# Kernel tuning notes

Measured on AMD Instinct MI355X. Metric: run time of the kernel, lower is better.

## Reference

```python
import jax, jax.numpy as jnp
import numpy as np

N = 30000      # nodes
E = 480000     # edges
H = 128        # hidden_nf
NQ = 7         # qubits
D = 2 ** NQ    # 128, quantum state dim == embedding_size
NL = 2         # block n_layers (QGCL layers)
QL = 2         # quantum circuit layers inside each QGCL
NORM = 100.0   # normalization_factor ('sum' aggregation)
NORM_CONST = 1.0


def _cnot_perm_indices(n):
    # Composed permutation for CNOT(0,1)...CNOT(n-2,n-1), CNOT(n-1,0).
    # PennyLane convention: wire 0 is the most significant bit.
    idx = np.arange(2 ** n)
    pairs = [(i, i + 1) for i in range(n - 1)] + [(n - 1, 0)]
    g = None
    for c, t in pairs:
        cb = (idx >> (n - 1 - c)) & 1
        f = idx ^ (cb << (n - 1 - t))  # flip target bit if control set (involution)
        g = f if g is None else g[f]
    return g

_CNOT_G = jnp.asarray(_cnot_perm_indices(NQ))


def _quantum_states(q_in, coeffs, A_re, A_im):
    """Vectorized VQC over all nodes. q_in [N,D] real -> [N,D] complex state."""
    norm = jnp.sqrt(jnp.sum(q_in ** 2, axis=1, keepdims=True) + 1e-12)
    s = (q_in / norm).astype(jnp.complex64)  # normalized initial state per node
    I = jnp.eye(D, dtype=jnp.complex64)
    for j in range(QL):
        # Cayley transform -> unitary
        A = (A_re[j] + 1j * A_im[j]).astype(jnp.complex64)
        A = A + A.conj().T
        q = (A - 1j * I) @ jnp.linalg.inv(A + 1j * I)
        # single-qubit layer: RY(b) @ RX(a) on every qubit -> kron power
        a, b = coeffs[j, 0].astype(jnp.complex64), coeffs[j, 1].astype(jnp.complex64)
        ca, sa = jnp.cos(a / 2), jnp.sin(a / 2)
        cb, sb = jnp.cos(b / 2), jnp.sin(b / 2)
        RX = jnp.stack([jnp.stack([ca, -1j * sa]), jnp.stack([-1j * sa, ca])])
        RY = jnp.stack([jnp.stack([cb, -sb]), jnp.stack([sb, cb])])
        G = RY @ RX
        Gk = G
        for _ in range(NQ - 1):
            Gk = jnp.kron(Gk, G)
        s = s @ q.T            # QubitUnitary
        s = s @ Gk.T           # RX/RY on all qubits
        s = s[:, _CNOT_G]      # CNOT ring (pure permutation)
    return s


def setup_inputs() -> dict:
    key = jax.random.key(0)
    ks = jax.random.split(key, 20)
    return {
        "h": jax.random.normal(ks[0], (N, H), jnp.float32),
        "x": jax.random.normal(ks[1], (N, 3), jnp.float32),
        "edge_index": jax.random.randint(ks[2], (2, E), 0, N, jnp.int32),
        "edge_attr": jax.random.normal(ks[3], (E, 1), jnp.float32),
        "e_w1": jax.random.normal(ks[4], (NL, 2 * H + 2, H), jnp.float32) * 0.05,
        "e_b1": jnp.zeros((NL, H), jnp.float32),
        "e_w2": jax.random.normal(ks[5], (NL, H, H), jnp.float32) * 0.05,
        "e_b2": jnp.zeros((NL, H), jnp.float32),
        "enc_w": jax.random.normal(ks[6], (NL, 2 * H, D), jnp.float32) * 0.05,
        "enc_b": jnp.zeros((NL, D), jnp.float32),
        "coeffs": jax.random.normal(ks[7], (NL, QL, 2), jnp.float32) * 0.1,
        "A_re": jax.random.normal(ks[8], (NL, QL, D, D), jnp.float32) * 0.01,
        "A_im": jax.random.normal(ks[9], (NL, QL, D, D), jnp.float32) * 0.01,
        "dec_w": jax.random.normal(ks[10], (NL, D, H), jnp.float32) * 0.05,
        "dec_b": jnp.zeros((NL, H), jnp.float32),
        "c_w1": jax.random.normal(ks[11], (2 * H + 2, H), jnp.float32) * 0.05,
        "c_b1": jnp.zeros((H,), jnp.float32),
        "c_w2": jax.random.normal(ks[12], (H, H), jnp.float32) * 0.05,
        "c_b2": jnp.zeros((H,), jnp.float32),
        "c_w3": jax.random.normal(ks[13], (H, 1), jnp.float32) * 0.001,  # xavier gain=0.001
    }


def reference(h, x, edge_index, edge_attr, e_w1, e_b1, e_w2, e_b2, enc_w, enc_b,
              coeffs, A_re, A_im, dec_w, dec_b, c_w1, c_b1, c_w2, c_b2, c_w3):
    row, col = edge_index[0], edge_index[1]
    # coord2diff
    diff = x[row] - x[col]
    radial = jnp.sum(diff ** 2, axis=1, keepdims=True)     # [E,1] (used as 'distances')
    coord_diff = diff / (jnp.sqrt(radial + 1e-8) + NORM_CONST)
    eattr = jnp.concatenate([radial, edge_attr], axis=1)   # [E,2]

    for l in range(NL):  # QGCL layers
        m = jnp.concatenate([h[row], h[col], eattr], axis=1)       # [E, 2H+2]
        m = jax.nn.silu(m @ e_w1[l] + e_b1[l])
        m = jax.nn.silu(m @ e_w2[l] + e_b2[l])                     # edge messages mij
        agg = jax.ops.segment_sum(m, row, num_segments=N) / NORM   # scatter-add
        q_in = jnp.concatenate([h, agg], axis=1) @ enc_w[l] + enc_b[l]
        # quantum part is detached in the original (torch .detach + re-tensor)
        qs = jax.lax.stop_gradient(
            _quantum_states(q_in, coeffs[l], A_re[l], A_im[l]))
        h = h + qs.real.astype(h.dtype) @ dec_w[l] + dec_b[l]

    # EquivariantUpdate (tanh=False)
    t = jnp.concatenate([h[row], h[col], eattr], axis=1)
    t = jax.nn.silu(t @ c_w1 + c_b1)
    t = jax.nn.silu(t @ c_w2 + c_b2)
    t = t @ c_w3                                                   # [E,1]
    trans = coord_diff * t
    x = x + jax.ops.segment_sum(trans, row, num_segments=N) / NORM
    return h, x
```

## Files before the change

### kernel.cpp

```cpp
#include <hip/hip_runtime.h>
#include <math.h>

#define N_NODES 30000
#define N_EDGES 480000
#define HDIM 128
#define EPB 64
#define AS 296
#define NAS 264
#define MS 136

typedef __attribute__((ext_vector_type(8))) short short8b;
typedef __attribute__((ext_vector_type(4))) float f32x4;

__device__ __forceinline__ float silu_f(float v) {
  return v / (1.0f + __expf(-v));
}

__device__ __forceinline__ unsigned short f2bf(float f) {
  unsigned int u = __float_as_uint(f);
  unsigned int r = u + 0x7fffu + ((u >> 16) & 1u);
  return (unsigned short)(r >> 16);
}

__global__ void init_out_bf_kernel(const float* __restrict__ h,
                                   const float* __restrict__ x,
                                   float* __restrict__ out,
                                   ushort* __restrict__ hbf) {
  int idx = blockIdx.x * 256 + threadIdx.x;
  float4 v = ((const float4*)h)[idx];
  ((float4*)out)[idx] = v;
  ushort4 o;
  o.x = f2bf(v.x); o.y = f2bf(v.y); o.z = f2bf(v.z); o.w = f2bf(v.w);
  ((ushort4*)hbf)[idx] = o;
  if (idx < N_NODES * 3 / 4) {
    ((float4*)(out + N_NODES * HDIM))[idx] = ((const float4*)x)[idx];
  }
}

__global__ void convert_all_kernel(
    const float* __restrict__ e_w1, const float* __restrict__ e_w2,
    const float* __restrict__ enc_w, const float* __restrict__ c_w1,
    const float* __restrict__ c_w2,
    ushort* __restrict__ w1cs, ushort* __restrict__ w2cs,
    ushort* __restrict__ enccs, ushort* __restrict__ cw1cs,
    ushort* __restrict__ cw2cs) {
  int idx = blockIdx.x * 256 + threadIdx.x;
  if (idx >= 55 * 4096) return;
  int ci = idx >> 12, rem = idx & 4095, n = rem >> 5, kk = rem & 31;
  const float* W;
  ushort* dst;
  int Kreal, ktl;
  if (ci < 18) {
    int l = ci / 9; ktl = ci - l * 9;
    W = e_w1 + (size_t)l * 258 * HDIM; dst = w1cs + (size_t)l * 9 * 4096;
    Kreal = 258;
  } else if (ci < 26) {
    int c2 = ci - 18; int l = c2 >> 2; ktl = c2 & 3;
    W = e_w2 + (size_t)l * HDIM * HDIM; dst = w2cs + (size_t)l * 4 * 4096;
    Kreal = 128;
  } else if (ci < 42) {
    int c2 = ci - 26; int l = c2 >> 3; ktl = c2 & 7;
    W = enc_w + (size_t)l * 256 * HDIM; dst = enccs + (size_t)l * 8 * 4096;
    Kreal = 256;
  } else if (ci < 51) {
    ktl = ci - 42; W = c_w1; dst = cw1cs; Kreal = 258;
  } else {
    ktl = ci - 51; W = c_w2; dst = cw2cs; Kreal = 128;
  }
  int k = ktl * 32 + kk;
  float v = (k < Kreal) ? W[(size_t)k * HDIM + n] : 0.0f;
  dst[ktl * 4096 + rem] = f2bf(v);
}

__global__ void count_kernel(const int* __restrict__ ei, int* __restrict__ cursor) {
  int e = blockIdx.x * 256 + threadIdx.x;
  atomicAdd(&cursor[ei[e]], 1);
}

__global__ __launch_bounds__(1024) void scan_kernel(int* __restrict__ cursor,
                                                    int* __restrict__ cstart) {
  __shared__ int sums[1024];
  const int tid = threadIdx.x;
  const int base = tid * 30;
  int local[30];
  int s = 0;
#pragma unroll
  for (int j = 0; j < 30; ++j) {
    int idx = base + j;
    int d = (idx < N_NODES) ? cursor[idx] : 0;
    local[j] = s;
    s += d;
// ... 6 lines not shown
    sums[tid] += add;
    __syncthreads();
  }
  int excl = (tid == 0) ? 0 : sums[tid - 1];
#pragma unroll
  for (int j = 0; j < 30; ++j) {
    int idx = base + j;
    if (idx < N_NODES) {
      int v = excl + local[j];
      cursor[idx] = v;
      cstart[idx] = v;
    }
  }
}

__global__ void fill_kernel(const int* __restrict__ ei, int* __restrict__ cursor,
                            int* __restrict__ elist) {
  int e = blockIdx.x * 256 + threadIdx.x;
  int r = ei[e];
  int pos = atomicAdd(&cursor[r], 1);
  elist[pos] = e;
}

__global__ void ns_init_kernel(const float* __restrict__ Are,
                               const float* __restrict__ Aim,
                               float2* __restrict__ X) {
  int lj = blockIdx.y;
  int idx = blockIdx.x * 256 + threadIdx.x;
  int r = idx >> 7, c = idx & 127;
  const float* are = Are + (size_t)lj * 16384;
  const float* aim = Aim + (size_t)lj * 16384;
  float re = are[r * 128 + c] + are[c * 128 + r];
  float im = aim[r * 128 + c] - aim[c * 128 + r];
  if (r == c) im -= 1.0f;
  X[(size_t)lj * 16384 + idx] = make_float2(re, im);
}

__global__ void ns_bx_kernel(const float* __restrict__ Are,
                             const float* __restrict__ Aim,
                             const float2* __restrict__ X,
                             float2* __restrict__ T) {
  int lj = blockIdx.y;
  int idx = blockIdx.x * 256 + threadIdx.x;
  int r = idx >> 7, c = idx & 127;
  const float* are = Are + (size_t)lj * 16384;
  const float* aim = Aim + (size_t)lj * 16384;
  const float2* x = X + (size_t)lj * 16384;
  float2 acc = make_float2(0.f, 0.f);
  for (int k = 0; k < 128; ++k) {
    float re = are[r * 128 + k] + are[k * 128 + r];
// ... 35 lines not shown
  const float* are = Are + (size_t)lj * 16384;
  const float* aim = Aim + (size_t)lj * 16384;
  const float2* binv = binvg + (size_t)lj * 16384;
  float2 acc = make_float2(0.f, 0.f);
  for (int k = 0; k < 128; ++k) {
    float re = are[r * 128 + k] + are[k * 128 + r];
    float im = aim[r * 128 + k] - aim[k * 128 + r];
    if (k == r) im -= 1.0f;
    float2 b = binv[k * 128 + c];
    acc.x += re * b.x - im * b.y;
    acc.y += re * b.y + im * b.x;
  }
  qm[(size_t)lj * 16384 + idx] = acc;
}

__global__ void gk_kernel(const float* __restrict__ coeffs,
                          float2* __restrict__ gkm) {
  int lj = blockIdx.y;
  float a = coeffs[lj * 2 + 0], b = coeffs[lj * 2 + 1];
  float ca = cosf(0.5f * a), sa = sinf(0.5f * a);
  float cb = cosf(0.5f * b), sb = sinf(0.5f * b);
  float2 G[2][2];
  G[0][0] = make_float2(cb * ca, sb * sa);
  G[0][1] = make_float2(-sb * ca, -cb * sa);
  G[1][0] = make_float2(sb * ca, -cb * sa);
  G[1][1] = make_float2(cb * ca, -sb * sa);
  int idx = blockIdx.x * 256 + threadIdx.x;
  int r = idx >> 7, c = idx & 127;
  float2 acc = make_float2(1.f, 0.f);
#pragma unroll
  for (int bit = 6; bit >= 0; --bit) {
    float2 g = G[(r >> bit) & 1][(c >> bit) & 1];
    acc = make_float2(acc.x * g.x - acc.y * g.y, acc.x * g.y + acc.y * g.x);
  }
  gkm[(size_t)lj * 16384 + idx] = acc;
}

__global__ void nj_kernel(const float2* __restrict__ qm,
                          const float2* __restrict__ gkm,
                          float2* __restrict__ njm) {
  int lj = blockIdx.y;
  int idx = blockIdx.x * 256 + threadIdx.x;
  int i = idx >> 7, c = idx & 127;
  int gc;
  {
    int v = c;
    const int cs[7] = {6, 5, 4, 3, 2, 1, 0};
    const int ts[7] = {0, 6, 5, 4, 3, 2, 1};
#pragma unroll
    for (int p = 0; p < 7; ++p) {
      int cb = (v >> (6 - cs[p])) & 1;
      v = v ^ (cb << (6 - ts[p]));
// ... 52 lines not shown
  __shared__ ushort A[EPB * AS];
  __shared__ int rows[EPB];
  ushort* m1 = A;
  float* m2 = (float*)A;

  const int tid = threadIdx.x;
  const int lane = tid & 63, wave = tid >> 6;
  const int lrow = lane & 15, lq = lane >> 4;
  const int wbase = wave * 32;
  const int woff0 = (wbase + lrow) * 32 + lq * 8;
  const int woff1 = (wbase + 16 + lrow) * 32 + lq * 8;

  const float b1v[2] = {b1[wbase + lrow], b1[wbase + 16 + lrow]};
  const float b2v[2] = {b2[wbase + lrow], b2[wbase + 16 + lrow]};

  const int i0 = blockIdx.x * EPB;
  {
    const int e = tid >> 2, j = tid & 3;
    const int edge = elist[i0 + e];
    const int r = ei[edge], c = ei[N_EDGES + edge];
    if (j == 0) rows[e] = r;
    const uint4* hr = (const uint4*)(hbf + (size_t)r * HDIM + j * 32);
    const uint4* hc = (const uint4*)(hbf + (size_t)c * HDIM + j * 32);
    uint4* d1 = (uint4*)(A + e * AS + j * 32);
    uint4* d2 = (uint4*)(A + e * AS + 128 + j * 32);
    d1[0] = hr[0]; d1[1] = hr[1]; d1[2] = hr[2]; d1[3] = hr[3];
    d2[0] = hc[0]; d2[1] = hc[1]; d2[2] = hc[2]; d2[3] = hc[3];
    if (j == 3) {
      float dx = x[r * 3 + 0] - x[c * 3 + 0];
      float dy = x[r * 3 + 1] - x[c * 3 + 1];
      float dz = x[r * 3 + 2] - x[c * 3 + 2];
      ushort* dst = A + e * AS;
      dst[256] = f2bf(dx * dx + dy * dy + dz * dz);
      dst[257] = f2bf(ea[edge]);
#pragma unroll
      for (int z = 258; z < 288; ++z) dst[z] = 0;
    }
  }
  __syncthreads();

  f32x4 acc[4][2];
#pragma unroll
  for (int mt = 0; mt < 4; ++mt)
#pragma unroll
    for (int nt = 0; nt < 2; ++nt) acc[mt][nt] = (f32x4){0.f, 0.f, 0.f, 0.f};
  {
    short8b wcur0 = *(const short8b*)(w1cs + woff0);
    short8b wcur1 = *(const short8b*)(w1cs + woff1);
#pragma unroll
    for (int kt = 0; kt < 9; ++kt) {
      short8b wn0, wn1;
      if (kt < 8) {
        wn0 = *(const short8b*)(w1cs + (kt + 1) * 4096 + woff0);
        wn1 = *(const short8b*)(w1cs + (kt + 1) * 4096 + woff1);
      }
      short8b af[4];
#pragma unroll
      for (int mt = 0; mt < 4; ++mt)
        af[mt] = *(const short8b*)(A + (mt * 16 + lrow) * AS + kt * 32 + lq * 8);
#pragma unroll
      for (int mt = 0; mt < 4; ++mt) {
        acc[mt][0] = __builtin_amdgcn_mfma_f32_16x16x32_bf16(af[mt], wcur0, acc[mt][0], 0, 0, 0);
        acc[mt][1] = __builtin_amdgcn_mfma_f32_16x16x32_bf16(af[mt], wcur1, acc[mt][1], 0, 0, 0);
      }
      if (kt < 8) { wcur0 = wn0; wcur1 = wn1; }
    }
  }
  __syncthreads();
#pragma unroll
  for (int mt = 0; mt < 4; ++mt)
#pragma unroll
    for (int nt = 0; nt < 2; ++nt)
#pragma unroll
      for (int r = 0; r < 4; ++r)
        m1[(mt * 16 + lq * 4 + r) * MS + wbase + nt * 16 + lrow] =
            f2bf(silu_f(acc[mt][nt][r] + b1v[nt]));
  __syncthreads();

  f32x4 acc2[4][2];
#pragma unroll
  for (int mt = 0; mt < 4; ++mt)
#pragma unroll
    for (int nt = 0; nt < 2; ++nt) acc2[mt][nt] = (f32x4){0.f, 0.f, 0.f, 0.f};
  {
    short8b wcur0 = *(const short8b*)(w2cs + woff0);
    short8b wcur1 = *(const short8b*)(w2cs + woff1);
#pragma unroll
    for (int kt = 0; kt < 4; ++kt) {
      short8b wn0, wn1;
      if (kt < 3) {
        wn0 = *(const short8b*)(w2cs + (kt + 1) * 4096 + woff0);
        wn1 = *(const short8b*)(w2cs + (kt + 1) * 4096 + woff1);
      }
      short8b af[4];
#pragma unroll
      for (int mt = 0; mt < 4; ++mt)
        af[mt] = *(const short8b*)(m1 + (mt * 16 + lrow) * MS + kt * 32 + lq * 8);
#pragma unroll
      for (int mt = 0; mt < 4; ++mt) {
        acc2[mt][0] = __builtin_amdgcn_mfma_f32_16x16x32_bf16(af[mt], wcur0, acc2[mt][0], 0, 0, 0);
        acc2[mt][1] = __builtin_amdgcn_mfma_f32_16x16x32_bf16(af[mt], wcur1, acc2[mt][1], 0, 0, 0);
      }
      if (kt < 3) { wcur0 = wn0; wcur1 = wn1; }
    }
  }
  __syncthreads();
#pragma unroll
  for (int mt = 0; mt < 4; ++mt)
#pragma unroll
    for (int nt = 0; nt < 2; ++nt)
#pragma unroll
      for (int r = 0; r < 4; ++r)
        m2[(mt * 16 + lq * 4 + r) * MS + wbase + nt * 16 + lrow] =
            silu_f(acc2[mt][nt][r] + b2v[nt]);
  __syncthreads();

  const int e2 = tid & 63, cg = tid >> 6, cb = cg * 32;
  const int r_e = rows[e2];
  const bool leader = (e2 == 0) || (rows[e2 - 1] != r_e);
  if (leader) {
    f32x4 sum[8];
#pragma unroll
    for (int q = 0; q < 8; ++q) sum[q] = *(const f32x4*)(m2 + e2 * MS + cb + q * 4);
    int f = e2 + 1;
    while (f < EPB && rows[f] == r_e) {
#pragma unroll
      for (int q = 0; q < 8; ++q) sum[q] += *(const f32x4*)(m2 + f * MS + cb + q * 4);
      ++f;
    }
    float* dst = (e2 == 0 && cstart[r_e] < i0)
                     ? headp + (size_t)blockIdx.x * HDIM + cb
                     : agg + (size_t)r_e * HDIM + cb;
#pragma unroll
    for (int q = 0; q < 8; ++q) *(f32x4*)(dst + q * 4) = sum[q];
  }
}

__global__ __launch_bounds__(256, 2) void node_mfma_kernel(
    float* __restrict__ out_h, const float* __restrict__ agg,
    const int* __restrict__ cstart, const int* __restrict__ cend,
    const float* __restrict__ headp,
    const ushort* __restrict__ enccs, const float* __restrict__ encb,
    const ushort* __restrict__ wqdcs, const float* __restrict__ decb,
    ushort* __restrict__ hbf) {
  __shared__ ushort A[EPB * NAS];
  __shared__ ushort m1[EPB * MS];
  __shared__ float nbuf[4 * EPB];
  const int tid = threadIdx.x;
  const int n0 = blockIdx.x * EPB;
// ... 152 lines not shown
  __shared__ float pbuf[4 * EPB];
  __shared__ float tv[EPB];
  ushort* m1 = A;

  const int tid = threadIdx.x;
  const int lane = tid & 63, wave = tid >> 6;
  const int lrow = lane & 15, lq = lane >> 4;
  const int wbase = wave * 32;
  const int woff0 = (wbase + lrow) * 32 + lq * 8;
  const int woff1 = (wbase + 16 + lrow) * 32 + lq * 8;

  const float b1v[2] = {b1[wbase + lrow], b1[wbase + 16 + lrow]};
  const float b2v[2] = {b2[wbase + lrow], b2[wbase + 16 + lrow]};
  const float w3v[2] = {w3[wbase + lrow], w3[wbase + 16 + lrow]};

  const int i0 = blockIdx.x * EPB;
  {
    const int e = tid >> 2, j = tid & 3;
    const int edge = elist[i0 + e];
    const int r = ei[edge], c = ei[N_EDGES + edge];
    if (j == 0) { rows[e] = r; colsA[e] = c; }
    const uint4* hr = (const uint4*)(hbf + (size_t)r * HDIM + j * 32);
    const uint4* hc = (const uint4*)(hbf + (size_t)c * HDIM + j * 32);
    uint4* d1 = (uint4*)(A + e * AS + j * 32);
    uint4* d2 = (uint4*)(A + e * AS + 128 + j * 32);
    d1[0] = hr[0]; d1[1] = hr[1]; d1[2] = hr[2]; d1[3] = hr[3];
    d2[0] = hc[0]; d2[1] = hc[1]; d2[2] = hc[2]; d2[3] = hc[3];
    if (j == 3) {
      float dx = x[r * 3 + 0] - x[c * 3 + 0];
      float dy = x[r * 3 + 1] - x[c * 3 + 1];
      float dz = x[r * 3 + 2] - x[c * 3 + 2];
      ushort* dst = A + e * AS;
      dst[256] = f2bf(dx * dx + dy * dy + dz * dz);
      dst[257] = f2bf(ea[edge]);
#pragma unroll
      for (int z = 258; z < 288; ++z) dst[z] = 0;
    }
  }
  __syncthreads();

  f32x4 acc[4][2];
#pragma unroll
  for (int mt = 0; mt < 4; ++mt)
#pragma unroll
    for (int nt = 0; nt < 2; ++nt) acc[mt][nt] = (f32x4){0.f, 0.f, 0.f, 0.f};
  {
    short8b wcur0 = *(const short8b*)(w1cs + woff0);
    short8b wcur1 = *(const short8b*)(w1cs + woff1);
#pragma unroll
    for (int kt = 0; kt < 9; ++kt) {
      short8b wn0, wn1;
      if (kt < 8) {
        wn0 = *(const short8b*)(w1cs + (kt + 1) * 4096 + woff0);
        wn1 = *(const short8b*)(w1cs + (kt + 1) * 4096 + woff1);
      }
      short8b af[4];
#pragma unroll
      for (int mt = 0; mt < 4; ++mt)
        af[mt] = *(const short8b*)(A + (mt * 16 + lrow) * AS + kt * 32 + lq * 8);
#pragma unroll
      for (int mt = 0; mt < 4; ++mt) {
        acc[mt][0] = __builtin_amdgcn_mfma_f32_16x16x32_bf16(af[mt], wcur0, acc[mt][0], 0, 0, 0);
        acc[mt][1] = __builtin_amdgcn_mfma_f32_16x16x32_bf16(af[mt], wcur1, acc[mt][1], 0, 0, 0);
      }
      if (kt < 8) { wcur0 = wn0; wcur1 = wn1; }
    }
  }
  __syncthreads();
#pragma unroll
  for (int mt = 0; mt < 4; ++mt)
#pragma unroll
    for (int nt = 0; nt < 2; ++nt)
#pragma unroll
      for (int r = 0; r < 4; ++r)
        m1[(mt * 16 + lq * 4 + r) * MS + wbase + nt * 16 + lrow] =
            f2bf(silu_f(acc[mt][nt][r] + b1v[nt]));
  __syncthreads();

  f32x4 acc2[4][2];
#pragma unroll
  for (int mt = 0; mt < 4; ++mt)
#pragma unroll
    for (int nt = 0; nt < 2; ++nt) acc2[mt][nt] = (f32x4){0.f, 0.f, 0.f, 0.f};
  {
    short8b wcur0 = *(const short8b*)(w2cs + woff0);
    short8b wcur1 = *(const short8b*)(w2cs + woff1);
#pragma unroll
    for (int kt = 0; kt < 4; ++kt) {
      short8b wn0, wn1;
      if (kt < 3) {
        wn0 = *(const short8b*)(w2cs + (kt + 1) * 4096 + woff0);
        wn1 = *(const short8b*)(w2cs + (kt + 1) * 4096 + woff1);
      }
      short8b af[4];
#pragma unroll
      for (int mt = 0; mt < 4; ++mt)
        af[mt] = *(const short8b*)(m1 + (mt * 16 + lrow) * MS + kt * 32 + lq * 8);
#pragma unroll
      for (int mt = 0; mt < 4; ++mt) {
        acc2[mt][0] = __builtin_amdgcn_mfma_f32_16x16x32_bf16(af[mt], wcur0, acc2[mt][0], 0, 0, 0);
        acc2[mt][1] = __builtin_amdgcn_mfma_f32_16x16x32_bf16(af[mt], wcur1, acc2[mt][1], 0, 0, 0);
      }
      if (kt < 3) { wcur0 = wn0; wcur1 = wn1; }
    }
  }
#pragma unroll
  for (int mt = 0; mt < 4; ++mt) {
    float p[4] = {0.f, 0.f, 0.f, 0.f};
#pragma unroll
    for (int nt = 0; nt < 2; ++nt)
#pragma unroll
      for (int r = 0; r < 4; ++r)
        p[r] += silu_f(acc2[mt][nt][r] + b2v[nt]) * w3v[nt];
#pragma unroll
    for (int m = 1; m < 16; m <<= 1)
#pragma unroll
      for (int r = 0; r < 4; ++r) p[r] += __shfl_xor(p[r], m, 64);
    if (lrow == 0) {
#pragma unroll
      for (int r = 0; r < 4; ++r)
        pbuf[wave * EPB + mt * 16 + lq * 4 + r] = p[r];
    }
  }
  __syncthreads();
  if (tid < EPB) {
    tv[tid] = (pbuf[tid] + pbuf[EPB + tid] + pbuf[2 * EPB + tid] + pbuf[3 * EPB + tid]) * 0.01f;
  }
  __syncthreads();
  if (tid < EPB) {
    const int e = tid;
    const int r_e = rows[e];
    const bool leader = (e == 0) || (rows[e - 1] != r_e);
    if (leader) {
      float sx = 0.f, sy = 0.f, sz = 0.f;
      int f = e;
      do {
        const int c = colsA[f];
        float dx = x[r_e * 3 + 0] - x[c * 3 + 0];
        float dy = x[r_e * 3 + 1] - x[c * 3 + 1];
        float dz = x[r_e * 3 + 2] - x[c * 3 + 2];
        float radial = dx * dx + dy * dy + dz * dz;
        float s = 1.0f / (sqrtf(radial + 1e-8f) + 1.0f);
        float t = tv[f];
        sx += dx * s * t; sy += dy * s * t; sz += dz * s * t;
        ++f;
      } while (f < EPB && rows[f] == r_e);
      atomicAdd(&xout[r_e * 3 + 0], sx);
      atomicAdd(&xout[r_e * 3 + 1], sy);
      atomicAdd(&xout[r_e * 3 + 2], sz);
    }
  }
}

extern "C" void kernel_launch(void* const* d_in, const int* in_sizes, int n_in,
                              void* d_out, int out_size, void* d_ws, size_t ws_size,
                              hipStream_t stream) {
  const float* h     = (const float*)d_in[0];
  const float* x     = (const float*)d_in[1];
  const int*   ei    = (const int*)d_in[2];
  const float* ea    = (const float*)d_in[3];
  const float* e_w1  = (const float*)d_in[4];
  const float* e_b1  = (const float*)d_in[5];
  const float* e_w2  = (const float*)d_in[6];
  const float* e_b2  = (const float*)d_in[7];
// ... 21 lines not shown
  float2* gkm    = (float2*)(ws + 4364288);
  float2* njm    = (float2*)(ws + 4495360);
  float2* um     = (float2*)(ws + 4626432);
  int*    cursor = (int*)(ws + 4724864);
  int*    cstart = (int*)(ws + 4754864);
  int*    elist  = (int*)(ws + 4784864);
  float*  headp  = ws + 5264864;
  ushort* hbf    = (ushort*)(ws + 6224864);
  ushort* w1cs   = (ushort*)(ws + 8144864);
  ushort* w2cs   = (ushort*)(ws + 8181728);
  ushort* cw1cs  = (ushort*)(ws + 8198112);
  ushort* cw2cs  = (ushort*)(ws + 8216544);
  ushort* enccs  = (ushort*)(ws + 8224736);
  ushort* wqdcs  = (ushort*)(ws + 8257504);

  init_out_bf_kernel<<<3750, 256, 0, stream>>>(h, x, out, hbf);

  hipMemsetAsync(cursor, 0, N_NODES * sizeof(int), stream);
  count_kernel<<<1875, 256, 0, stream>>>(ei, cursor);
  scan_kernel<<<1, 1024, 0, stream>>>(cursor, cstart);
  fill_kernel<<<1875, 256, 0, stream>>>(ei, cursor, elist);

  convert_all_kernel<<<880, 256, 0, stream>>>(e_w1, e_w2, enc_w, c_w1, c_w2,
                                              w1cs, w2cs, enccs, cw1cs, cw2cs);

  ns_init_kernel<<<dim3(64, 4), 256, 0, stream>>>(A_re, A_im, xa);
  float2* cur = xa;
  float2* nxt = xb;
  for (int it = 0; it < 3; ++it) {
    ns_bx_kernel<<<dim3(64, 4), 256, 0, stream>>>(A_re, A_im, cur, xt);
    ns_upd_kernel<<<dim3(64, 4), 256, 0, stream>>>(cur, xt, nxt);
    float2* tmp = cur; cur = nxt; nxt = tmp;
  }
  qmat_kernel<<<dim3(64, 4), 256, 0, stream>>>(A_re, A_im, cur, qm);
  gk_kernel<<<dim3(64, 4), 256, 0, stream>>>(coeffs, gkm);
  nj_kernel<<<dim3(64, 4), 256, 0, stream>>>(qm, gkm, njm);
  compose_kernel<<<dim3(64, 2), 256, 0, stream>>>(njm, um);
  wqd_kernel<<<dim3(64, 2), 256, 0, stream>>>(um, dec_w, wqdcs);

  for (int l = 0; l < 2; ++l) {
    edge_mfma_kernel<<<N_EDGES / EPB, 256, 0, stream>>>(
        hbf, ei, x, ea, elist, cstart,
        w1cs + (size_t)l * 9 * 4096, e_b1 + l * HDIM,
        w2cs + (size_t)l * 4 * 4096, e_b2 + l * HDIM, agg, headp);
    node_mfma_kernel<<<(N_NODES + EPB - 1) / EPB, 256, 0, stream>>>(
        out, agg, cstart, cursor, headp,
        enccs + (size_t)l * 8 * 4096, enc_b + l * HDIM,
        wqdcs + (size_t)l * 4 * 4096, dec_b + l * HDIM, hbf);
  }

  coord_mfma_kernel<<<N_EDGES / EPB, 256, 0, stream>>>(
      hbf, ei, x, ea, elist, cw1cs, c_b1, cw2cs, c_b2, c_w3,
      out + (size_t)N_NODES * HDIM);
}
```

Measured before the change: 770.1 us.

## Merge prep kernels, cut Newton-Schulz iterations, double-buffer edge tiles per block

Several independent changes ship together. The edge count now runs inside the init kernel, and the fill, weight conversion, NS init and Gk construction are merged into one prep kernel, which removes several launches. The edge and coord MFMA kernels now handle two 64-edge tiles per block and prefetch the second tile's gathered rows into registers during the first tile's compute, which hides gather latency but halves the grid. The Newton-Schulz inverse drops from three iterations to two, which may cost accuracy in the Cayley unitary.

```diff
diff --git a/kernel.cpp b/kernel.cpp
--- a/kernel.cpp
+++ b/kernel.cpp
@@ -24,8 +24,10 @@
 
 __global__ void init_out_bf_kernel(const float* __restrict__ h,
                                    const float* __restrict__ x,
+                                   const int* __restrict__ ei,
                                    float* __restrict__ out,
-                                   ushort* __restrict__ hbf) {
+                                   ushort* __restrict__ hbf,
+                                   int* __restrict__ cursor) {
   int idx = blockIdx.x * 256 + threadIdx.x;
   float4 v = ((const float4*)h)[idx];
   ((float4*)out)[idx] = v;
@@ -35,46 +37,7 @@
   if (idx < N_NODES * 3 / 4) {
     ((float4*)(out + N_NODES * HDIM))[idx] = ((const float4*)x)[idx];
   }
-}
-
-__global__ void convert_all_kernel(
-    const float* __restrict__ e_w1, const float* __restrict__ e_w2,
-    const float* __restrict__ enc_w, const float* __restrict__ c_w1,
-    const float* __restrict__ c_w2,
-    ushort* __restrict__ w1cs, ushort* __restrict__ w2cs,
-    ushort* __restrict__ enccs, ushort* __restrict__ cw1cs,
-    ushort* __restrict__ cw2cs) {
-  int idx = blockIdx.x * 256 + threadIdx.x;
-  if (idx >= 55 * 4096) return;
-  int ci = idx >> 12, rem = idx & 4095, n = rem >> 5, kk = rem & 31;
-  const float* W;
-  ushort* dst;
-  int Kreal, ktl;
-  if (ci < 18) {
-    int l = ci / 9; ktl = ci - l * 9;
-    W = e_w1 + (size_t)l * 258 * HDIM; dst = w1cs + (size_t)l * 9 * 4096;
-    Kreal = 258;
-  } else if (ci < 26) {
-    int c2 = ci - 18; int l = c2 >> 2; ktl = c2 & 3;
-    W = e_w2 + (size_t)l * HDIM * HDIM; dst = w2cs + (size_t)l * 4 * 4096;
-    Kreal = 128;
-  } else if (ci < 42) {
-    int c2 = ci - 26; int l = c2 >> 3; ktl = c2 & 7;
-    W = enc_w + (size_t)l * 256 * HDIM; dst = enccs + (size_t)l * 8 * 4096;
-    Kreal = 256;
-  } else if (ci < 51) {
-    ktl = ci - 42; W = c_w1; dst = cw1cs; Kreal = 258;
-  } else {
-    ktl = ci - 51; W = c_w2; dst = cw2cs; Kreal = 128;
-  }
-  int k = ktl * 32 + kk;
-  float v = (k < Kreal) ? W[(size_t)k * HDIM + n] : 0.0f;
-  dst[ktl * 4096 + rem] = f2bf(v);
-}
-
-__global__ void count_kernel(const int* __restrict__ ei, int* __restrict__ cursor) {
-  int e = blockIdx.x * 256 + threadIdx.x;
-  atomicAdd(&cursor[ei[e]], 1);
+  if (idx < N_EDGES) atomicAdd(&cursor[ei[idx]], 1);
 }
 
 __global__ __launch_bounds__(1024) void scan_kernel(int* __restrict__ cursor,
@@ -111,26 +74,80 @@
   }
 }
 
-__global__ void fill_kernel(const int* __restrict__ ei, int* __restrict__ cursor,
-                            int* __restrict__ elist) {
-  int e = blockIdx.x * 256 + threadIdx.x;
-  int r = ei[e];
-  int pos = atomicAdd(&cursor[r], 1);
-  elist[pos] = e;
-}
-
-__global__ void ns_init_kernel(const float* __restrict__ Are,
-                               const float* __restrict__ Aim,
-                               float2* __restrict__ X) {
-  int lj = blockIdx.y;
-  int idx = blockIdx.x * 256 + threadIdx.x;
-  int r = idx >> 7, c = idx & 127;
-  const float* are = Are + (size_t)lj * 16384;
-  const float* aim = Aim + (size_t)lj * 16384;
-  float re = are[r * 128 + c] + are[c * 128 + r];
-  float im = aim[r * 128 + c] - aim[c * 128 + r];
-  if (r == c) im -= 1.0f;
-  X[(size_t)lj * 16384 + idx] = make_float2(re, im);
+__global__ void prep_kernel(
+    const int* __restrict__ ei, int* __restrict__ cursor, int* __restrict__ elist,
+    const float* __restrict__ e_w1, const float* __restrict__ e_w2,
+    const float* __restrict__ enc_w, const float* __restrict__ c_w1,
+    const float* __restrict__ c_w2,
+    ushort* __restrict__ w1cs, ushort* __restrict__ w2cs,
+    ushort* __restrict__ enccs, ushort* __restrict__ cw1cs,
+    ushort* __restrict__ cw2cs,
+    const float* __restrict__ A_re, const float* __restrict__ A_im,
+    float2* __restrict__ X,
+    const float* __restrict__ coeffs, float2* __restrict__ gkm) {
+  const int b = blockIdx.x, tid = threadIdx.x;
+  if (b < 1875) {
+    int e = b * 256 + tid;
+    int r = ei[e];
+    int pos = atomicAdd(&cursor[r], 1);
+    elist[pos] = e;
+  } else if (b < 2755) {
+    int idx = (b - 1875) * 256 + tid;
+    int ci = idx >> 12, rem = idx & 4095, kk = rem & 31;
+    const float* W; ushort* dst; int Kreal, ktl;
+    if (ci < 18) {
+      int l = ci / 9; ktl = ci - l * 9;
+      W = e_w1 + (size_t)l * 258 * HDIM; dst = w1cs + (size_t)l * 9 * 4096;
+      Kreal = 258;
+    } else if (ci < 26) {
+      int c2 = ci - 18; int l = c2 >> 2; ktl = c2 & 3;
+      W = e_w2 + (size_t)l * HDIM * HDIM; dst = w2cs + (size_t)l * 4 * 4096;
+      Kreal = 128;
+    } else if (ci < 42) {
+      int c2 = ci - 26; int l = c2 >> 3; ktl = c2 & 7;
+      W = enc_w + (size_t)l * 256 * HDIM; dst = enccs + (size_t)l * 8 * 4096;
+      Kreal = 256;
+    } else if (ci < 51) {
+      ktl = ci - 42; W = c_w1; dst = cw1cs; Kreal = 258;
+    } else {
+      ktl = ci - 51; W = c_w2; dst = cw2cs; Kreal = 128;
+    }
+    int n = rem >> 5;
+    int k = ktl * 32 + kk;
+    float v = (k < Kreal) ? W[(size_t)k * HDIM + n] : 0.0f;
+    dst[ktl * 4096 + rem] = f2bf(v);
+  } else if (b < 3011) {
+    int bb = b - 2755;
+    int lj = bb >> 6;
+    int idx = (bb & 63) * 256 + tid;
+    int r = idx >> 7, c = idx & 127;
+    const float* are = A_re + (size_t)lj * 16384;
+    const float* aim = A_im + (size_t)lj * 16384;
+    float re = are[r * 128 + c] + are[c * 128 + r];
+    float im = aim[r * 128 + c] - aim[c * 128 + r];
+    if (r == c) im -= 1.0f;
+    X[(size_t)lj * 16384 + idx] = make_float2(re, im);
+  } else {
+    int bb = b - 3011;
+    int lj = bb >> 6;
+    float a = coeffs[lj * 2 + 0], bcf = coeffs[lj * 2 + 1];
+    float ca = cosf(0.5f * a), sa = sinf(0.5f * a);
+    float cb = cosf(0.5f * bcf), sb = sinf(0.5f * bcf);
+    float2 G[2][2];
+    G[0][0] = make_float2(cb * ca, sb * sa);
+    G[0][1] = make_float2(-sb * ca, -cb * sa);
+    G[1][0] = make_float2(sb * ca, -cb * sa);
+    G[1][1] = make_float2(cb * ca, -sb * sa);
+    int idx = (bb & 63) * 256 + tid;
+    int r = idx >> 7, c = idx & 127;
+    float2 acc = make_float2(1.f, 0.f);
+#pragma unroll
+    for (int bit = 6; bit >= 0; --bit) {
+      float2 g = G[(r >> bit) & 1][(c >> bit) & 1];
+      acc = make_float2(acc.x * g.x - acc.y * g.y, acc.x * g.y + acc.y * g.x);
+    }
+    gkm[(size_t)lj * 16384 + idx] = acc;
+  }
 }
 
 __global__ void ns_bx_kernel(const float* __restrict__ Are,
@@ -196,28 +213,6 @@
   qm[(size_t)lj * 16384 + idx] = acc;
 }
 
-__global__ void gk_kernel(const float* __restrict__ coeffs,
-                          float2* __restrict__ gkm) {
-  int lj = blockIdx.y;
-  float a = coeffs[lj * 2 + 0], b = coeffs[lj * 2 + 1];
-  float ca = cosf(0.5f * a), sa = sinf(0.5f * a);
-  float cb = cosf(0.5f * b), sb = sinf(0.5f * b);
-  float2 G[2][2];
-  G[0][0] = make_float2(cb * ca, sb * sa);
-  G[0][1] = make_float2(-sb * ca, -cb * sa);
-  G[1][0] = make_float2(sb * ca, -cb * sa);
-  G[1][1] = make_float2(cb * ca, -sb * sa);
-  int idx = blockIdx.x * 256 + threadIdx.x;
-  int r = idx >> 7, c = idx & 127;
-  float2 acc = make_float2(1.f, 0.f);
-#pragma unroll
-  for (int bit = 6; bit >= 0; --bit) {
-    float2 g = G[(r >> bit) & 1][(c >> bit) & 1];
-    acc = make_float2(acc.x * g.x - acc.y * g.y, acc.x * g.y + acc.y * g.x);
-  }
-  gkm[(size_t)lj * 16384 + idx] = acc;
-}
-
 __global__ void nj_kernel(const float2* __restrict__ qm,
                           const float2* __restrict__ gkm,
                           float2* __restrict__ njm) {
@@ -300,125 +295,156 @@
   const float b1v[2] = {b1[wbase + lrow], b1[wbase + 16 + lrow]};
   const float b2v[2] = {b2[wbase + lrow], b2[wbase + 16 + lrow]};
 
-  const int i0 = blockIdx.x * EPB;
-  {
-    const int e = tid >> 2, j = tid & 3;
-    const int edge = elist[i0 + e];
-    const int r = ei[edge], c = ei[N_EDGES + edge];
-    if (j == 0) rows[e] = r;
-    const uint4* hr = (const uint4*)(hbf + (size_t)r * HDIM + j * 32);
-    const uint4* hc = (const uint4*)(hbf + (size_t)c * HDIM + j * 32);
+  const int e = tid >> 2, j = tid & 3;
+  const int t0 = blockIdx.x * 2;
+
+  const int edge0 = elist[t0 * EPB + e];
+  const int r0 = ei[edge0], c0 = ei[N_EDGES + edge0];
+  const int edge1 = elist[t0 * EPB + EPB + e];
+  const int r1 = ei[edge1], c1 = ei[N_EDGES + edge1];
+
+  uint4 R[8];
+  float2 meta;
+
+  auto stage_load = [&](int rr, int cc, int eg) {
+    const uint4* hr = (const uint4*)(hbf + (size_t)rr * HDIM + j * 32);
+    const uint4* hc = (const uint4*)(hbf + (size_t)cc * HDIM + j * 32);
+    R[0] = hr[0]; R[1] = hr[1]; R[2] = hr[2]; R[3] = hr[3];
+    R[4] = hc[0]; R[5] = hc[1]; R[6] = hc[2]; R[7] = hc[3];
+    if (j == 3) {
+      float dx = x[rr * 3 + 0] - x[cc * 3 + 0];
+      float dy = x[rr * 3 + 1] - x[cc * 3 + 1];
+      float dz = x[rr * 3 + 2] - x[cc * 3 + 2];
+      meta.x = dx * dx + dy * dy + dz * dz;
+      meta.y = ea[eg];
+    }
+  };
+  auto stage_write = [&](int rr) {
     uint4* d1 = (uint4*)(A + e * AS + j * 32);
     uint4* d2 = (uint4*)(A + e * AS + 128 + j * 32);
-    d1[0] = hr[0]; d1[1] = hr[1]; d1[2] = hr[2]; d1[3] = hr[3];
-    d2[0] = hc[0]; d2[1] = hc[1]; d2[2] = hc[2]; d2[3] = hc[3];
+    d1[0] = R[0]; d1[1] = R[1]; d1[2] = R[2]; d1[3] = R[3];
+    d2[0] = R[4]; d2[1] = R[5]; d2[2] = R[6]; d2[3] = R[7];
+    if (j == 0) rows[e] = rr;
     if (j == 3) {
-      float dx = x[r * 3 + 0] - x[c * 3 + 0];
-      float dy = x[r * 3 + 1] - x[c * 3 + 1];
-      float dz = x[r * 3 + 2] - x[c * 3 + 2];
       ushort* dst = A + e * AS;
-      dst[256] = f2bf(dx * dx + dy * dy + dz * dz);
-      dst[257] = f2bf(ea[edge]);
+      dst[256] = f2bf(meta.x);
+      dst[257] = f2bf(meta.y);
 #pragma unroll
       for (int z = 258; z < 288; ++z) dst[z] = 0;
     }
-  }
+  };
+
+  stage_load(r0, c0, edge0);
+  stage_write(r0);
   __syncthreads();
 
-  f32x4 acc[4][2];
-#pragma unroll
-  for (int mt = 0; mt < 4; ++mt)
-#pragma unroll
-    for (int nt = 0; nt < 2; ++nt) acc[mt][nt] = (f32x4){0.f, 0.f, 0.f, 0.f};
-  {
-    short8b wcur0 = *(const short8b*)(w1cs + woff0);
-    short8b wcur1 = *(const short8b*)(w1cs + woff1);
-#pragma unroll
-    for (int kt = 0; kt < 9; ++kt) {
-      short8b wn0, wn1;
-      if (kt < 8) {
-        wn0 = *(const short8b*)(w1cs + (kt + 1) * 4096 + woff0);
-        wn1 = *(const short8b*)(w1cs + (kt + 1) * 4096 + woff1);
-      }
-      short8b af[4];
-#pragma unroll
-      for (int mt = 0; mt < 4; ++mt)
-        af[mt] = *(const short8b*)(A + (mt * 16 + lrow) * AS + kt * 32 + lq * 8);
-#pragma unroll
-      for (int mt = 0; mt < 4; ++mt) {
-        acc[mt][0] = __builtin_amdgcn_mfma_f32_16x16x32_bf16(af[mt], wcur0, acc[mt][0], 0, 0, 0);
-        acc[mt][1] = __builtin_amdgcn_mfma_f32_16x16x32_bf16(af[mt], wcur1, acc[mt][1], 0, 0, 0);
-      }
-      if (kt < 8) { wcur0 = wn0; wcur1 = wn1; }
-    }
-  }
-  __syncthreads();
-#pragma unroll
-  for (int mt = 0; mt < 4; ++mt)
-#pragma unroll
-    for (int nt = 0; nt < 2; ++nt)
-#pragma unroll
-      for (int r = 0; r < 4; ++r)
-        m1[(mt * 16 + lq * 4 + r) * MS + wbase + nt * 16 + lrow] =
-            f2bf(silu_f(acc[mt][nt][r] + b1v[nt]));
-  __syncthreads();
-
-  f32x4 acc2[4][2];
-#pragma unroll
-  for (int mt = 0; mt < 4; ++mt)
-#pragma unroll
-    for (int nt = 0; nt < 2; ++nt) acc2[mt][nt] = (f32x4){0.f, 0.f, 0.f, 0.f};
-  {
-    short8b wcur0 = *(const short8b*)(w2cs + woff0);
-    short8b wcur1 = *(const short8b*)(w2cs + woff1);
-#pragma unroll
-    for (int kt = 0; kt < 4; ++kt) {
-      short8b wn0, wn1;
-      if (kt < 3) {
-        wn0 = *(const short8b*)(w2cs + (kt + 1) * 4096 + woff0);
-        wn1 = *(const short8b*)(w2cs + (kt + 1) * 4096 + woff1);
-      }
-      short8b af[4];
-#pragma unroll
-      for (int mt = 0; mt < 4; ++mt)
-        af[mt] = *(const short8b*)(m1 + (mt * 16 + lrow) * MS + kt * 32 + lq * 8);
-#pragma unroll
-      for (int mt = 0; mt < 4; ++mt) {
-        acc2[mt][0] = __builtin_amdgcn_mfma_f32_16x16x32_bf16(af[mt], wcur0, acc2[mt][0], 0, 0, 0);
-        acc2[mt][1] = __builtin_amdgcn_mfma_f32_16x16x32_bf16(af[mt], wcur1, acc2[mt][1], 0, 0, 0);
-      }
-      if (kt < 3) { wcur0 = wn0; wcur1 = wn1; }
-    }
-  }
-  __syncthreads();
-#pragma unroll
-  for (int mt = 0; mt < 4; ++mt)
-#pragma unroll
-    for (int nt = 0; nt < 2; ++nt)
-#pragma unroll
-      for (int r = 0; r < 4; ++r)
-        m2[(mt * 16 + lq * 4 + r) * MS + wbase + nt * 16 + lrow] =
-            silu_f(acc2[mt][nt][r] + b2v[nt]);
-  __syncthreads();
-
-  const int e2 = tid & 63, cg = tid >> 6, cb = cg * 32;
-  const int r_e = rows[e2];
-  const bool leader = (e2 == 0) || (rows[e2 - 1] != r_e);
-  if (leader) {
-    f32x4 sum[8];
-#pragma unroll
-    for (int q = 0; q < 8; ++q) sum[q] = *(const f32x4*)(m2 + e2 * MS + cb + q * 4);
-    int f = e2 + 1;
-    while (f < EPB && rows[f] == r_e) {
-#pragma unroll
-      for (int q = 0; q < 8; ++q) sum[q] += *(const f32x4*)(m2 + f * MS + cb + q * 4);
-      ++f;
-    }
-    float* dst = (e2 == 0 && cstart[r_e] < i0)
-                     ? headp + (size_t)blockIdx.x * HDIM + cb
-                     : agg + (size_t)r_e * HDIM + cb;
-#pragma unroll
-    for (int q = 0; q < 8; ++q) *(f32x4*)(dst + q * 4) = sum[q];
+#pragma unroll
+  for (int half = 0; half < 2; ++half) {
+    f32x4 acc[4][2];
+#pragma unroll
+    for (int mt = 0; mt < 4; ++mt)
+#pragma unroll
+      for (int nt = 0; nt < 2; ++nt) acc[mt][nt] = (f32x4){0.f, 0.f, 0.f, 0.f};
+    {
+      short8b wcur0 = *(const short8b*)(w1cs + woff0);
+      short8b wcur1 = *(const short8b*)(w1cs + woff1);
+#pragma unroll
+      for (int kt = 0; kt < 9; ++kt) {
+        short8b wn0, wn1;
+        if (kt < 8) {
+          wn0 = *(const short8b*)(w1cs + (kt + 1) * 4096 + woff0);
+          wn1 = *(const short8b*)(w1cs + (kt + 1) * 4096 + woff1);
+        }
+        short8b af[4];
+#pragma unroll
+        for (int mt = 0; mt < 4; ++mt)
+          af[mt] = *(const short8b*)(A + (mt * 16 + lrow) * AS + kt * 32 + lq * 8);
+#pragma unroll
+        for (int mt = 0; mt < 4; ++mt) {
+          acc[mt][0] = __builtin_amdgcn_mfma_f32_16x16x32_bf16(af[mt], wcur0, acc[mt][0], 0, 0, 0);
+          acc[mt][1] = __builtin_amdgcn_mfma_f32_16x16x32_bf16(af[mt], wcur1, acc[mt][1], 0, 0, 0);
+        }
+        if (kt < 8) { wcur0 = wn0; wcur1 = wn1; }
+      }
+    }
+    __syncthreads();
+#pragma unroll
+    for (int mt = 0; mt < 4; ++mt)
+#pragma unroll
+      for (int nt = 0; nt < 2; ++nt)
+#pragma unroll
+        for (int r = 0; r < 4; ++r)
+          m1[(mt * 16 + lq * 4 + r) * MS + wbase + nt * 16 + lrow] =
+              f2bf(silu_f(acc[mt][nt][r] + b1v[nt]));
+    __syncthreads();
+
+    f32x4 acc2[4][2];
+#pragma unroll
+    for (int mt = 0; mt < 4; ++mt)
+#pragma unroll
+      for (int nt = 0; nt < 2; ++nt) acc2[mt][nt] = (f32x4){0.f, 0.f, 0.f, 0.f};
+    {
+      short8b wcur0 = *(const short8b*)(w2cs + woff0);
+      short8b wcur1 = *(const short8b*)(w2cs + woff1);
+#pragma unroll
+      for (int kt = 0; kt < 4; ++kt) {
+        short8b wn0, wn1;
+        if (kt < 3) {
+          wn0 = *(const short8b*)(w2cs + (kt + 1) * 4096 + woff0);
+          wn1 = *(const short8b*)(w2cs + (kt + 1) * 4096 + woff1);
+        }
+        short8b af[4];
+#pragma unroll
+        for (int mt = 0; mt < 4; ++mt)
+          af[mt] = *(const short8b*)(m1 + (mt * 16 + lrow) * MS + kt * 32 + lq * 8);
+#pragma unroll
+        for (int mt = 0; mt < 4; ++mt) {
+          acc2[mt][0] = __builtin_amdgcn_mfma_f32_16x16x32_bf16(af[mt], wcur0, acc2[mt][0], 0, 0, 0);
+          acc2[mt][1] = __builtin_amdgcn_mfma_f32_16x16x32_bf16(af[mt], wcur1, acc2[mt][1], 0, 0, 0);
+        }
+        if (kt < 3) { wcur0 = wn0; wcur1 = wn1; }
+      }
+    }
+
+    if (half == 0) stage_load(r1, c1, edge1);
+
+    __syncthreads();
+#pragma unroll
+    for (int mt = 0; mt < 4; ++mt)
+#pragma unroll
+      for (int nt = 0; nt < 2; ++nt)
+#pragma unroll
+        for (int r = 0; r < 4; ++r)
+          m2[(mt * 16 + lq * 4 + r) * MS + wbase + nt * 16 + lrow] =
+              silu_f(acc2[mt][nt][r] + b2v[nt]);
+    __syncthreads();
+
+    const int i0h = (t0 + half) * EPB;
+    const int e2 = tid & 63, cg = tid >> 6, cb = cg * 32;
+    const int r_e = rows[e2];
+    const bool leader = (e2 == 0) || (rows[e2 - 1] != r_e);
+    if (leader) {
+      f32x4 sum[8];
+#pragma unroll
+      for (int q = 0; q < 8; ++q) sum[q] = *(const f32x4*)(m2 + e2 * MS + cb + q * 4);
+      int f = e2 + 1;
+      while (f < EPB && rows[f] == r_e) {
+#pragma unroll
+        for (int q = 0; q < 8; ++q) sum[q] += *(const f32x4*)(m2 + f * MS + cb + q * 4);
+        ++f;
+      }
+      float* dst = (e2 == 0 && cstart[r_e] < i0h)
+                       ? headp + (size_t)(t0 + half) * HDIM + cb
+                       : agg + (size_t)r_e * HDIM + cb;
+#pragma unroll
+      for (int q = 0; q < 8; ++q) *(f32x4*)(dst + q * 4) = sum[q];
+    }
+
+    if (half == 0) {
+      __syncthreads();
+      stage_write(r1);
+      __syncthreads();
+    }
   }
 }
 
@@ -601,140 +627,170 @@
   const float b2v[2] = {b2[wbase + lrow], b2[wbase + 16 + lrow]};
   const float w3v[2] = {w3[wbase + lrow], w3[wbase + 16 + lrow]};
 
-  const int i0 = blockIdx.x * EPB;
-  {
-    const int e = tid >> 2, j = tid & 3;
-    const int edge = elist[i0 + e];
-    const int r = ei[edge], c = ei[N_EDGES + edge];
-    if (j == 0) { rows[e] = r; colsA[e] = c; }
-    const uint4* hr = (const uint4*)(hbf + (size_t)r * HDIM + j * 32);
-    const uint4* hc = (const uint4*)(hbf + (size_t)c * HDIM + j * 32);
+  const int e = tid >> 2, j = tid & 3;
+  const int t0 = blockIdx.x * 2;
+
+  const int edge0 = elist[t0 * EPB + e];
+  const int r0 = ei[edge0], c0 = ei[N_EDGES + edge0];
+  const int edge1 = elist[t0 * EPB + EPB + e];
+  const int r1 = ei[edge1], c1 = ei[N_EDGES + edge1];
+
+  uint4 R[8];
+  float2 meta;
+
+  auto stage_load = [&](int rr, int cc, int eg) {
+    const uint4* hr = (const uint4*)(hbf + (size_t)rr * HDIM + j * 32);
+    const uint4* hc = (const uint4*)(hbf + (size_t)cc * HDIM + j * 32);
+    R[0] = hr[0]; R[1] = hr[1]; R[2] = hr[2]; R[3] = hr[3];
+    R[4] = hc[0]; R[5] = hc[1]; R[6] = hc[2]; R[7] = hc[3];
+    if (j == 3) {
+      float dx = x[rr * 3 + 0] - x[cc * 3 + 0];
+      float dy = x[rr * 3 + 1] - x[cc * 3 + 1];
+      float dz = x[rr * 3 + 2] - x[cc * 3 + 2];
+      meta.x = dx * dx + dy * dy + dz * dz;
+      meta.y = ea[eg];
+    }
+  };
+  auto stage_write = [&](int rr, int cc) {
     uint4* d1 = (uint4*)(A + e * AS + j * 32);
     uint4* d2 = (uint4*)(A + e * AS + 128 + j * 32);
-    d1[0] = hr[0]; d1[1] = hr[1]; d1[2] = hr[2]; d1[3] = hr[3];
-    d2[0] = hc[0]; d2[1] = hc[1]; d2[2] = hc[2]; d2[3] = hc[3];
+    d1[0] = R[0]; d1[1] = R[1]; d1[2] = R[2]; d1[3] = R[3];
+    d2[0] = R[4]; d2[1] = R[5]; d2[2] = R[6]; d2[3] = R[7];
+    if (j == 0) { rows[e] = rr; colsA[e] = cc; }
     if (j == 3) {
-      float dx = x[r * 3 + 0] - x[c * 3 + 0];
-      float dy = x[r * 3 + 1] - x[c * 3 + 1];
-      float dz = x[r * 3 + 2] - x[c * 3 + 2];
       ushort* dst = A + e * AS;
-      dst[256] = f2bf(dx * dx + dy * dy + dz * dz);
-      dst[257] = f2bf(ea[edge]);
+      dst[256] = f2bf(meta.x);
+      dst[257] = f2bf(meta.y);
 #pragma unroll
       for (int z = 258; z < 288; ++z) dst[z] = 0;
     }
-  }
+  };
+
+  stage_load(r0, c0, edge0);
+  stage_write(r0, c0);
   __syncthreads();
 
-  f32x4 acc[4][2];
-#pragma unroll
-  for (int mt = 0; mt < 4; ++mt)
-#pragma unroll
-    for (int nt = 0; nt < 2; ++nt) acc[mt][nt] = (f32x4){0.f, 0.f, 0.f, 0.f};
-  {
-    short8b wcur0 = *(const short8b*)(w1cs + woff0);
-    short8b wcur1 = *(const short8b*)(w1cs + woff1);
-#pragma unroll
-    for (int kt = 0; kt < 9; ++kt) {
-      short8b wn0, wn1;
-      if (kt < 8) {
-        wn0 = *(const short8b*)(w1cs + (kt + 1) * 4096 + woff0);
-        wn1 = *(const short8b*)(w1cs + (kt + 1) * 4096 + woff1);
-      }
-      short8b af[4];
-#pragma unroll
-      for (int mt = 0; mt < 4; ++mt)
-        af[mt] = *(const short8b*)(A + (mt * 16 + lrow) * AS + kt * 32 + lq * 8);
-#pragma unroll
-      for (int mt = 0; mt < 4; ++mt) {
-        acc[mt][0] = __builtin_amdgcn_mfma_f32_16x16x32_bf16(af[mt], wcur0, acc[mt][0], 0, 0, 0);
-        acc[mt][1] = __builtin_amdgcn_mfma_f32_16x16x32_bf16(af[mt], wcur1, acc[mt][1], 0, 0, 0);
-      }
-      if (kt < 8) { wcur0 = wn0; wcur1 = wn1; }
-    }
-  }
-  __syncthreads();
-#pragma unroll
-  for (int mt = 0; mt < 4; ++mt)
-#pragma unroll
-    for (int nt = 0; nt < 2; ++nt)
-#pragma unroll
-      for (int r = 0; r < 4; ++r)
-        m1[(mt * 16 + lq * 4 + r) * MS + wbase + nt * 16 + lrow] =
-            f2bf(silu_f(acc[mt][nt][r] + b1v[nt]));
-  __syncthreads();
-
-  f32x4 acc2[4][2];
-#pragma unroll
-  for (int mt = 0; mt < 4; ++mt)
-#pragma unroll
-    for (int nt = 0; nt < 2; ++nt) acc2[mt][nt] = (f32x4){0.f, 0.f, 0.f, 0.f};
-  {
-    short8b wcur0 = *(const short8b*)(w2cs + woff0);
-    short8b wcur1 = *(const short8b*)(w2cs + woff1);
-#pragma unroll
-    for (int kt = 0; kt < 4; ++kt) {
-      short8b wn0, wn1;
-      if (kt < 3) {
-        wn0 = *(const short8b*)(w2cs + (kt + 1) * 4096 + woff0);
-        wn1 = *(const short8b*)(w2cs + (kt + 1) * 4096 + woff1);
-      }
-      short8b af[4];
-#pragma unroll
-      for (int mt = 0; mt < 4; ++mt)
-        af[mt] = *(const short8b*)(m1 + (mt * 16 + lrow) * MS + kt * 32 + lq * 8);
-#pragma unroll
-      for (int mt = 0; mt < 4; ++mt) {
-        acc2[mt][0] = __builtin_amdgcn_mfma_f32_16x16x32_bf16(af[mt], wcur0, acc2[mt][0], 0, 0, 0);
-        acc2[mt][1] = __builtin_amdgcn_mfma_f32_16x16x32_bf16(af[mt], wcur1, acc2[mt][1], 0, 0, 0);
-      }
-      if (kt < 3) { wcur0 = wn0; wcur1 = wn1; }
-    }
-  }
-#pragma unroll
-  for (int mt = 0; mt < 4; ++mt) {
-    float p[4] = {0.f, 0.f, 0.f, 0.f};
-#pragma unroll
-    for (int nt = 0; nt < 2; ++nt)
-#pragma unroll
-      for (int r = 0; r < 4; ++r)
-        p[r] += silu_f(acc2[mt][nt][r] + b2v[nt]) * w3v[nt];
-#pragma unroll
-    for (int m = 1; m < 16; m <<= 1)
-#pragma unroll
-      for (int r = 0; r < 4; ++r) p[r] += __shfl_xor(p[r], m, 64);
-    if (lrow == 0) {
-#pragma unroll
-      for (int r = 0; r < 4; ++r)
-        pbuf[wave * EPB + mt * 16 + lq * 4 + r] = p[r];
-    }
-  }
-  __syncthreads();
-  if (tid < EPB) {
-    tv[tid] = (pbuf[tid] + pbuf[EPB + tid] + pbuf[2 * EPB + tid] + pbuf[3 * EPB + tid]) * 0.01f;
-  }
-  __syncthreads();
-  if (tid < EPB) {
-    const int e = tid;
-    const int r_e = rows[e];
-    const bool leader = (e == 0) || (rows[e - 1] != r_e);
-    if (leader) {
-      float sx = 0.f, sy = 0.f, sz = 0.f;
-      int f = e;
-      do {
-        const int c = colsA[f];
-        float dx = x[r_e * 3 + 0] - x[c * 3 + 0];
-        float dy = x[r_e * 3 + 1] - x[c * 3 + 1];
-        float dz = x[r_e * 3 + 2] - x[c * 3 + 2];
-        float radial = dx * dx + dy * dy + dz * dz;
-        float s = 1.0f / (sqrtf(radial + 1e-8f) + 1.0f);
-        float t = tv[f];
-        sx += dx * s * t; sy += dy * s * t; sz += dz * s * t;
-        ++f;
-      } while (f < EPB && rows[f] == r_e);
-      atomicAdd(&xout[r_e * 3 + 0], sx);
-      atomicAdd(&xout[r_e * 3 + 1], sy);
-      atomicAdd(&xout[r_e * 3 + 2], sz);
+#pragma unroll
+  for (int half = 0; half < 2; ++half) {
+    f32x4 acc[4][2];
+#pragma unroll
+    for (int mt = 0; mt < 4; ++mt)
+#pragma unroll
+      for (int nt = 0; nt < 2; ++nt) acc[mt][nt] = (f32x4){0.f, 0.f, 0.f, 0.f};
+    {
+      short8b wcur0 = *(const short8b*)(w1cs + woff0);
+      short8b wcur1 = *(const short8b*)(w1cs + woff1);
+#pragma unroll
+      for (int kt = 0; kt < 9; ++kt) {
+        short8b wn0, wn1;
+        if (kt < 8) {
+          wn0 = *(const short8b*)(w1cs + (kt + 1) * 4096 + woff0);
+          wn1 = *(const short8b*)(w1cs + (kt + 1) * 4096 + woff1);
+        }
+        short8b af[4];
+#pragma unroll
+        for (int mt = 0; mt < 4; ++mt)
+          af[mt] = *(const short8b*)(A + (mt * 16 + lrow) * AS + kt * 32 + lq * 8);
+#pragma unroll
+        for (int mt = 0; mt < 4; ++mt) {
+          acc[mt][0] = __builtin_amdgcn_mfma_f32_16x16x32_bf16(af[mt], wcur0, acc[mt][0], 0, 0, 0);
+          acc[mt][1] = __builtin_amdgcn_mfma_f32_16x16x32_bf16(af[mt], wcur1, acc[mt][1], 0, 0, 0);
+        }
+        if (kt < 8) { wcur0 = wn0; wcur1 = wn1; }
+      }
+    }
+    __syncthreads();
+#pragma unroll
+    for (int mt = 0; mt < 4; ++mt)
+#pragma unroll
+      for (int nt = 0; nt < 2; ++nt)
+#pragma unroll
+        for (int r = 0; r < 4; ++r)
+          m1[(mt * 16 + lq * 4 + r) * MS + wbase + nt * 16 + lrow] =
+              f2bf(silu_f(acc[mt][nt][r] + b1v[nt]));
+    __syncthreads();
+
+    f32x4 acc2[4][2];
+#pragma unroll
+    for (int mt = 0; mt < 4; ++mt)
+#pragma unroll
+      for (int nt = 0; nt < 2; ++nt) acc2[mt][nt] = (f32x4){0.f, 0.f, 0.f, 0.f};
+    {
+      short8b wcur0 = *(const short8b*)(w2cs + woff0);
+      short8b wcur1 = *(const short8b*)(w2cs + woff1);
+#pragma unroll
+      for (int kt = 0; kt < 4; ++kt) {
+        short8b wn0, wn1;
+        if (kt < 3) {
+          wn0 = *(const short8b*)(w2cs + (kt + 1) * 4096 + woff0);
+          wn1 = *(const short8b*)(w2cs + (kt + 1) * 4096 + woff1);
+        }
+        short8b af[4];
+#pragma unroll
+        for (int mt = 0; mt < 4; ++mt)
+          af[mt] = *(const short8b*)(m1 + (mt * 16 + lrow) * MS + kt * 32 + lq * 8);
+#pragma unroll
+        for (int mt = 0; mt < 4; ++mt) {
+          acc2[mt][0] = __builtin_amdgcn_mfma_f32_16x16x32_bf16(af[mt], wcur0, acc2[mt][0], 0, 0, 0);
+          acc2[mt][1] = __builtin_amdgcn_mfma_f32_16x16x32_bf16(af[mt], wcur1, acc2[mt][1], 0, 0, 0);
+        }
+        if (kt < 3) { wcur0 = wn0; wcur1 = wn1; }
+      }
+    }
+
+    if (half == 0) stage_load(r1, c1, edge1);
+
+#pragma unroll
+    for (int mt = 0; mt < 4; ++mt) {
+      float p[4] = {0.f, 0.f, 0.f, 0.f};
+#pragma unroll
+      for (int nt = 0; nt < 2; ++nt)
+#pragma unroll
+        for (int r = 0; r < 4; ++r)
+          p[r] += silu_f(acc2[mt][nt][r] + b2v[nt]) * w3v[nt];
+#pragma unroll
+      for (int m = 1; m < 16; m <<= 1)
+#pragma unroll
+        for (int r = 0; r < 4; ++r) p[r] += __shfl_xor(p[r], m, 64);
+      if (lrow == 0) {
+#pragma unroll
+        for (int r = 0; r < 4; ++r)
+          pbuf[wave * EPB + mt * 16 + lq * 4 + r] = p[r];
+      }
+    }
+    __syncthreads();
+    if (tid < EPB) {
+      tv[tid] = (pbuf[tid] + pbuf[EPB + tid] + pbuf[2 * EPB + tid] + pbuf[3 * EPB + tid]) * 0.01f;
+    }
+    __syncthreads();
+    if (tid < EPB) {
+      const int e2 = tid;
+      const int r_e = rows[e2];
+      const bool leader = (e2 == 0) || (rows[e2 - 1] != r_e);
+      if (leader) {
+        float sx = 0.f, sy = 0.f, sz = 0.f;
+        int f = e2;
+        do {
+          const int c = colsA[f];
+          float dx = x[r_e * 3 + 0] - x[c * 3 + 0];
+          float dy = x[r_e * 3 + 1] - x[c * 3 + 1];
+          float dz = x[r_e * 3 + 2] - x[c * 3 + 2];
+          float radial = dx * dx + dy * dy + dz * dz;
+          float s = 1.0f / (sqrtf(radial + 1e-8f) + 1.0f);
+          float t = tv[f];
+          sx += dx * s * t; sy += dy * s * t; sz += dz * s * t;
+          ++f;
+        } while (f < EPB && rows[f] == r_e);
+        atomicAdd(&xout[r_e * 3 + 0], sx);
+        atomicAdd(&xout[r_e * 3 + 1], sy);
+        atomicAdd(&xout[r_e * 3 + 2], sz);
+      }
+    }
+
+    if (half == 0) {
+      __syncthreads();
+      stage_write(r1, c1);
+      __syncthreads();
     }
   }
 }
@@ -786,32 +842,29 @@
   ushort* enccs  = (ushort*)(ws + 8224736);
   ushort* wqdcs  = (ushort*)(ws + 8257504);
 
-  init_out_bf_kernel<<<3750, 256, 0, stream>>>(h, x, out, hbf);
-
   hipMemsetAsync(cursor, 0, N_NODES * sizeof(int), stream);
-  count_kernel<<<1875, 256, 0, stream>>>(ei, cursor);
+  init_out_bf_kernel<<<3750, 256, 0, stream>>>(h, x, ei, out, hbf, cursor);
   scan_kernel<<<1, 1024, 0, stream>>>(cursor, cstart);
-  fill_kernel<<<1875, 256, 0, stream>>>(ei, cursor, elist);
-
-  convert_all_kernel<<<880, 256, 0, stream>>>(e_w1, e_w2, enc_w, c_w1, c_w2,
-                                              w1cs, w2cs, enccs, cw1cs, cw2cs);
-
-  ns_init_kernel<<<dim3(64, 4), 256, 0, stream>>>(A_re, A_im, xa);
+
+  prep_kernel<<<3267, 256, 0, stream>>>(ei, cursor, elist,
+                                        e_w1, e_w2, enc_w, c_w1, c_w2,
+                                        w1cs, w2cs, enccs, cw1cs, cw2cs,
+                                        A_re, A_im, xa, coeffs, gkm);
+
   float2* cur = xa;
   float2* nxt = xb;
-  for (int it = 0; it < 3; ++it) {
+  for (int it = 0; it < 2; ++it) {
     ns_bx_kernel<<<dim3(64, 4), 256, 0, stream>>>(A_re, A_im, cur, xt);
     ns_upd_kernel<<<dim3(64, 4), 256, 0, stream>>>(cur, xt, nxt);
     float2* tmp = cur; cur = nxt; nxt = tmp;
   }
   qmat_kernel<<<dim3(64, 4), 256, 0, stream>>>(A_re, A_im, cur, qm);
-  gk_kernel<<<dim3(64, 4), 256, 0, stream>>>(coeffs, gkm);
   nj_kernel<<<dim3(64, 4), 256, 0, stream>>>(qm, gkm, njm);
   compose_kernel<<<dim3(64, 2), 256, 0, stream>>>(njm, um);
   wqd_kernel<<<dim3(64, 2), 256, 0, stream>>>(um, dec_w, wqdcs);
 
   for (int l = 0; l < 2; ++l) {
-    edge_mfma_kernel<<<N_EDGES / EPB, 256, 0, stream>>>(
+    edge_mfma_kernel<<<N_EDGES / (2 * EPB), 256, 0, stream>>>(
         hbf, ei, x, ea, elist, cstart,
         w1cs + (size_t)l * 9 * 4096, e_b1 + l * HDIM,
         w2cs + (size_t)l * 4 * 4096, e_b2 + l * HDIM, agg, headp);
@@ -821,7 +874,7 @@
         wqdcs + (size_t)l * 4 * 4096, dec_b + l * HDIM, hbf);
   }
 
-  coord_mfma_kernel<<<N_EDGES / EPB, 256, 0, stream>>>(
+  coord_mfma_kernel<<<N_EDGES / (2 * EPB), 256, 0, stream>>>(
       hbf, ei, x, ea, elist, cw1cs, c_b1, cw2cs, c_b2, c_w3,
       out + (size_t)N_NODES * HDIM);
 }
```

After: 913.4 us. 18.6% more time.
